# Kernel tuning notes

Hardware: AMD Instinct MI355X
Metric: run time of the kernel (lower is better)

The kernel has to match this reference:

```python
import jax, jax.numpy as jnp
import numpy as np

B = 8192
NUM_NODES = 100000
EMB = 128
W1D, W2D, W3D = 64, 128, 256   # witness_dims
CODE = 128
HID = 64                        # hardcoded hidden_dim in WitnessExtractor / decoder
TOTW = W1D + W2D + W3D          # 448


def _linear_params(key, fan_in, fan_out):
    k1, k2 = jax.random.split(key)
    bound = 1.0 / np.sqrt(fan_in)
    w = jax.random.uniform(k1, (fan_out, fan_in), jnp.float32, -bound, bound)
    b = jax.random.uniform(k2, (fan_out,), jnp.float32, -bound, bound)
    return w, b


def setup_inputs() -> dict:
    key = jax.random.key(0)
    ks = jax.random.split(key, 12)
    u = jax.random.randint(ks[0], (B,), 0, NUM_NODES, dtype=jnp.int64 if jax.config.jax_enable_x64 else jnp.int32)
    v = jax.random.randint(ks[1], (B,), 0, NUM_NODES, dtype=u.dtype)
    emb = jax.random.normal(ks[2], (NUM_NODES, EMB), jnp.float32)
    e1_w1, e1_b1 = _linear_params(ks[3], 2 * EMB, HID)
    e1_w2, e1_b2 = _linear_params(ks[4], HID, W1D)
    e2_w1, e2_b1 = _linear_params(ks[5], 2 * EMB + W1D, HID)
    e2_w2, e2_b2 = _linear_params(ks[6], HID, W2D)
    e3_w1, e3_b1 = _linear_params(ks[7], 2 * EMB + W2D, HID)
    e3_w2, e3_b2 = _linear_params(ks[8], HID, W3D)
    trop_w = jax.random.normal(ks[9], (CODE, TOTW), jnp.float32)  # init_scale=1.0
    dec_w1, dec_b1 = _linear_params(ks[10], CODE, HID)
    dec_w2, dec_b2 = _linear_params(ks[11], HID, 1)
    return dict(u=u, v=v, emb=emb,
                e1_w1=e1_w1, e1_b1=e1_b1, e1_w2=e1_w2, e1_b2=e1_b2,
                e2_w1=e2_w1, e2_b1=e2_b1, e2_w2=e2_w2, e2_b2=e2_b2,
                e3_w1=e3_w1, e3_b1=e3_b1, e3_w2=e3_w2, e3_b2=e3_b2,
                trop_w=trop_w, dec_w1=dec_w1, dec_b1=dec_b1,
                dec_w2=dec_w2, dec_b2=dec_b2)


def _witness(x, w1, b1, w2, b2):
    h = jax.nn.relu(x @ w1.T + b1)
    return jax.nn.sigmoid(h @ w2.T + b2)


def reference(u, v, emb,
              e1_w1, e1_b1, e1_w2, e1_b2,
              e2_w1, e2_b1, e2_w2, e2_b2,
              e3_w1, e3_b1, e3_w2, e3_b2,
              trop_w, dec_w1, dec_b1, dec_w2, dec_b2):
    u_emb = emb[u]                               # [B, EMB]
    v_emb = emb[v]
    base = jnp.concatenate([u_emb, v_emb], axis=1)  # [B, 2*EMB]
    w1 = _witness(base, e1_w1, e1_b1, e1_w2, e1_b2)
    w2 = _witness(jnp.concatenate([base, w1], axis=1), e2_w1, e2_b1, e2_w2, e2_b2)
    w3 = _witness(jnp.concatenate([base, w2], axis=1), e3_w1, e3_b1, e3_w2, e3_b2)
    wit = jnp.concatenate([w1, w2, w3], axis=1)  # [B, TOTW]
    # tropical (min-plus) matmul: code[b,o] = min_j (wit[b,j] + trop_w[o,j])
    code = jnp.min(wit[:, None, :] + trop_w[None, :, :], axis=2)  # [B, CODE]
    h = jax.nn.relu(code @ dec_w1.T + dec_b1)
    return h @ dec_w2.T + dec_b2                 # [B, 1]
```

## Files before the change

kernel.cpp:

```cpp
#include <hip/hip_runtime.h>
#include <hip/hip_fp16.h>
#include <math.h>

#define BATCH 8192
#define EMB 128
#define TILE 32
#define NTHREADS 1024
#define NWAVES 16

#define OFF_E1W1 0
#define OFF_E1W2 16384
#define OFF_E2W1 20480
#define OFF_E2W2 40960
#define OFF_E3W1 49152
#define OFF_E3W2 73728
#define OFF_TROP 90112
#define OFF_DW1  147456
#define OFF_DW2  155648
#define W_TOTAL  155712

typedef __attribute__((ext_vector_type(8))) _Float16 v8h;
typedef __attribute__((ext_vector_type(2))) _Float16 half2v;
typedef __attribute__((ext_vector_type(4))) float v4f;

struct Smem {
    _Float16 XB[32 * 32 * 8];
    _Float16 WIT[56 * 32 * 8];
    _Float16 H[8 * 32 * 8];
    _Float16 CODE[16 * 32 * 8];
};

static_assert(sizeof(Smem) == (32*32*8 + 56*32*8 + 8*32*8 + 16*32*8) * 2, "lds size");

__global__ __launch_bounds__(256) void cvt_weights_kernel(
    const float* __restrict__ s0, const float* __restrict__ s1,
    const float* __restrict__ s2, const float* __restrict__ s3,
    const float* __restrict__ s4, const float* __restrict__ s5,
    const float* __restrict__ s6, const float* __restrict__ s7,
    const float* __restrict__ s8, _Float16* __restrict__ ws)
{
    const int idx4 = (blockIdx.x * 256 + threadIdx.x) * 4;
    if (idx4 >= W_TOTAL) return;
    const float* src; int off;
    if      (idx4 < OFF_E1W2) { src = s0; off = OFF_E1W1; }
    else if (idx4 < OFF_E2W1) { src = s1; off = OFF_E1W2; }
    else if (idx4 < OFF_E2W2) { src = s2; off = OFF_E2W1; }
    else if (idx4 < OFF_E3W1) { src = s3; off = OFF_E2W2; }
    else if (idx4 < OFF_E3W2) { src = s4; off = OFF_E3W1; }
    else if (idx4 < OFF_TROP) { src = s5; off = OFF_E3W2; }
    else if (idx4 < OFF_DW1)  { src = s6; off = OFF_TROP; }
    else if (idx4 < OFF_DW2)  { src = s7; off = OFF_DW1;  }
    else                      { src = s8; off = OFF_DW2;  }
    const float4 v = *(const float4*)(src + (idx4 - off));
    _Float16* dst = ws + idx4;
    dst[0] = (_Float16)v.x;
    dst[1] = (_Float16)v.y;
    dst[2] = (_Float16)v.z;
    dst[3] = (_Float16)v.w;
}

template <int K, int STEPS0, int O, int ACT>
__device__ __forceinline__ void dense_mfma(
    const _Float16* __restrict__ Wg, const float* __restrict__ bias,
    const _Float16* A0, const _Float16* A1, _Float16* Out,
    int wave, int lane)
{
    constexpr int STEPS = K / 32;
    constexpr int NJOBS = 2 * (O / 16);
    constexpr int JLIM = (NJOBS < NWAVES) ? NWAVES : NJOBS;
    const int l15 = lane & 15;
    const int quad = lane >> 4;

    for (int job = wave; job < JLIM; job += NWAVES) {
        const int jid = job % NJOBS;
        const int mt = jid & 1;
        const int nt = jid >> 1;
        v4f c = {0.f, 0.f, 0.f, 0.f};
        const _Float16* wrow = Wg + (size_t)(nt * 16 + l15) * K + quad * 8;
        #pragma unroll
        for (int s = 0; s < STEPS; ++s) {
            const int g = s * 4 + quad;
            const _Float16* asrc = (s < STEPS0)
                ? (A0 + ((size_t)g * 32 + mt * 16 + l15) * 8)
                : (A1 + ((size_t)(g - STEPS0 * 4) * 32 + mt * 16 + l15) * 8);
            const v8h a = *(const v8h*)asrc;
            const v8h b = *(const v8h*)(wrow + s * 32);
            c = __builtin_amdgcn_mfma_f32_16x16x32_f16(a, b, c, 0, 0, 0);
        }
        const int o = nt * 16 + l15;
        const float bs = bias[o];
        #pragma unroll
        for (int i = 0; i < 4; ++i) {
            float vv = c[i] + bs;
            if (ACT == 0) vv = fmaxf(vv, 0.f);
            else          vv = 1.f / (1.f + __expf(-vv));
            const int m = mt * 16 + quad * 4 + i;
            Out[((o >> 3) * 32 + m) * 8 + (o & 7)] = (_Float16)vv;
        }
    }
}

__global__ __launch_bounds__(NTHREADS) void tacit_fused_kernel(
    const int* __restrict__ u, const int* __restrict__ v,
    const float* __restrict__ emb,
    const float* __restrict__ e1_b1, const float* __restrict__ e1_b2,
    const float* __restrict__ e2_b1, const float* __restrict__ e2_b2,
    const float* __restrict__ e3_b1, const float* __restrict__ e3_b2,
    const float* __restrict__ dec_b1, const float* __restrict__ dec_b2,
    const _Float16* __restrict__ ws,
    float* __restrict__ out)
{
    __shared__ Smem S;
    const int tid = threadIdx.x;
    const int lane = tid & 63;
    const int wave = tid >> 6;
    const int row0 = blockIdx.x * TILE;

    {
        const int row = tid & 31;
        const int kq = tid >> 5;
        const int node = (kq < 16) ? u[row0 + row] : v[row0 + row];
        const int col = (kq & 15) * 8;
        const float4 f0 = *(const float4*)(emb + (size_t)node * EMB + col);
        const float4 f1 = *(const float4*)(emb + (size_t)node * EMB + col + 4);
        v8h hv;
        hv[0] = (_Float16)f0.x; hv[1] = (_Float16)f0.y;
        hv[2] = (_Float16)f0.z; hv[3] = (_Float16)f0.w;
        hv[4] = (_Float16)f1.x; hv[5] = (_Float16)f1.y;
        hv[6] = (_Float16)f1.z; hv[7] = (_Float16)f1.w;
        *(v8h*)&S.XB[((size_t)kq * 32 + row) * 8] = hv;
    }
    __syncthreads();

    dense_mfma<256, 8, 64, 0>(ws + OFF_E1W1, e1_b1, S.XB, nullptr, S.H, wave, lane);
    __syncthreads();
    dense_mfma<64, 2, 64, 1>(ws + OFF_E1W2, e1_b2, S.H, nullptr, S.WIT, wave, lane);
    __syncthreads();

    dense_mfma<320, 8, 64, 0>(ws + OFF_E2W1, e2_b1, S.XB, S.WIT, S.H, wave, lane);
    __syncthreads();
    dense_mfma<64, 2, 128, 1>(ws + OFF_E2W2, e2_b2, S.H, nullptr, S.WIT + 8 * 256, wave, lane);
    __syncthreads();

    dense_mfma<384, 8, 64, 0>(ws + OFF_E3W1, e3_b1, S.XB, S.WIT + 8 * 256, S.H, wave, lane);
    __syncthreads();
    dense_mfma<64, 2, 256, 1>(ws + OFF_E3W2, e3_b2, S.H, nullptr, S.WIT + 24 * 256, wave, lane);
    __syncthreads();

    {
        const int g = wave >> 1;
        const int rh = wave & 1;
        const int l15 = lane & 15;
        const int sub = lane >> 4;
        const int o = g * 16 + l15;
        half2v acc[16];
        const half2v big = {(_Float16)60000.f, (_Float16)60000.f};
        #pragma unroll
        for (int r = 0; r < 16; ++r) acc[r] = big;
        const _Float16* Trow = ws + OFF_TROP + (size_t)o * 448 + sub * 112;
        #pragma unroll 2
        for (int c = 0; c < 14; ++c) {
            const float4 wr = *(const float4*)(Trow + c * 8);
            const half2v w0 = __builtin_bit_cast(half2v, wr.x);
            const half2v w1 = __builtin_bit_cast(half2v, wr.y);
            const half2v w2 = __builtin_bit_cast(half2v, wr.z);
            const half2v w3 = __builtin_bit_cast(half2v, wr.w);
            const int kq = sub * 14 + c;
            const _Float16* xb = &S.WIT[((size_t)kq * 32 + rh * 16) * 8];
            #pragma unroll
            for (int r = 0; r < 16; ++r) {
                const float4 xr = *(const float4*)(xb + r * 8);
                half2v t0 = __builtin_bit_cast(half2v, xr.x) + w0;
                half2v t1 = __builtin_bit_cast(half2v, xr.y) + w1;
                half2v t2 = __builtin_bit_cast(half2v, xr.z) + w2;
                half2v t3 = __builtin_bit_cast(half2v, xr.w) + w3;
                t0 = __builtin_elementwise_min(t0, t1);
                t2 = __builtin_elementwise_min(t2, t3);
                acc[r] = __builtin_elementwise_min(acc[r], __builtin_elementwise_min(t0, t2));
            }
        }
        #pragma unroll
        for (int r = 0; r < 16; ++r) {
            half2v v1 = __builtin_bit_cast(half2v,
                __shfl_xor(__builtin_bit_cast(int, acc[r]), 16, 64));
            acc[r] = __builtin_elementwise_min(acc[r], v1);
            half2v v2 = __builtin_bit_cast(half2v,
                __shfl_xor(__builtin_bit_cast(int, acc[r]), 32, 64));
            acc[r] = __builtin_elementwise_min(acc[r], v2);
        }
        if (sub == 0) {
            #pragma unroll
            for (int r = 0; r < 16; ++r) {
                const _Float16 lo = acc[r].x;
                const _Float16 hi = acc[r].y;
                S.CODE[((o >> 3) * 32 + rh * 16 + r) * 8 + (o & 7)] =
                    (lo < hi) ? lo : hi;
            }
        }
    }
    __syncthreads();

    dense_mfma<128, 4, 64, 0>(ws + OFF_DW1, dec_b1, S.CODE, nullptr, S.H, wave, lane);
    __syncthreads();

    if (tid < TILE) {
        const int r = tid;
        float s = dec_b2[0];
        const _Float16* w2 = ws + OFF_DW2;
        #pragma unroll
        for (int c = 0; c < 8; ++c) {
            const float4 hr = *(const float4*)(&S.H[((size_t)c * 32 + r) * 8]);
            const float4 wr = *(const float4*)(w2 + c * 8);
            s = __builtin_amdgcn_fdot2(__builtin_bit_cast(half2v, hr.x), __builtin_bit_cast(half2v, wr.x), s, false);
            s = __builtin_amdgcn_fdot2(__builtin_bit_cast(half2v, hr.y), __builtin_bit_cast(half2v, wr.y), s, false);
            s = __builtin_amdgcn_fdot2(__builtin_bit_cast(half2v, hr.z), __builtin_bit_cast(half2v, wr.z), s, false);
            s = __builtin_amdgcn_fdot2(__builtin_bit_cast(half2v, hr.w), __builtin_bit_cast(half2v, wr.w), s, false);
        }
        out[row0 + r] = s;
    }
}

extern "C" void kernel_launch(void* const* d_in, const int* in_sizes, int n_in,
                              void* d_out, int out_size, void* d_ws, size_t ws_size,
                              hipStream_t stream) {
    const int*   u      = (const int*)d_in[0];
    const int*   v      = (const int*)d_in[1];
    const float* emb    = (const float*)d_in[2];
    const float* e1_w1  = (const float*)d_in[3];
    const float* e1_b1  = (const float*)d_in[4];
    const float* e1_w2  = (const float*)d_in[5];
    const float* e1_b2  = (const float*)d_in[6];
    const float* e2_w1  = (const float*)d_in[7];
    const float* e2_b1  = (const float*)d_in[8];
    const float* e2_w2  = (const float*)d_in[9];
    const float* e2_b2  = (const float*)d_in[10];
    const float* e3_w1  = (const float*)d_in[11];
    const float* e3_b1  = (const float*)d_in[12];
    const float* e3_w2  = (const float*)d_in[13];
    const float* e3_b2  = (const float*)d_in[14];
    const float* trop_w = (const float*)d_in[15];
    const float* dec_w1 = (const float*)d_in[16];
    const float* dec_b1 = (const float*)d_in[17];
    const float* dec_w2 = (const float*)d_in[18];
    const float* dec_b2 = (const float*)d_in[19];
    float* out = (float*)d_out;
    _Float16* ws = (_Float16*)d_ws;

    const int cvt_blocks = (W_TOTAL / 4 + 255) / 256;
    cvt_weights_kernel<<<cvt_blocks, 256, 0, stream>>>(
        e1_w1, e1_w2, e2_w1, e2_w2, e3_w1, e3_w2, trop_w, dec_w1, dec_w2, ws);

    tacit_fused_kernel<<<BATCH / TILE, NTHREADS, 0, stream>>>(
        u, v, emb,
        e1_b1, e1_b2, e2_b1, e2_b2, e3_b1, e3_b2, dec_b1, dec_b2,
        ws, out);
}
```

Baseline: 161.6 us.

## Prune tropical weights to near-minimum entries and sparsify min-plus stage

A prep kernel finds each trop_w row's minimum and keeps only entries within about 1.02 of it, stored as a compact (index, fp16 value) list with row offsets in the workspace. This is exact because the sigmoid witnesses lie in (0,1), so a pruned entry can never be the minimum. The dense min-plus loop over all 448 columns becomes a short sparse scan over a row-major witness copy in LDS. The batch tile also shrinks to 16 rows with a padded LDS stride and an occupancy hint. Risks: many waves sit idle in the small dense layers, and a fixed entry cap (4096) could truncate unusual weight sets.

```diff
diff --git a/kernel.cpp b/kernel.cpp
--- a/kernel.cpp
+++ b/kernel.cpp
@@ -4,9 +4,12 @@
 
 #define BATCH 8192
 #define EMB 128
-#define TILE 32
+#define TILE 16
 #define NTHREADS 1024
 #define NWAVES 16
+#define CH 136
+#define WITS 450
+#define ENT_CAP 4096
 
 #define OFF_E1W1 0
 #define OFF_E1W2 16384
@@ -14,78 +17,111 @@
 #define OFF_E2W2 40960
 #define OFF_E3W1 49152
 #define OFF_E3W2 73728
-#define OFF_TROP 90112
-#define OFF_DW1  147456
-#define OFF_DW2  155648
-#define W_TOTAL  155712
+#define OFF_DW1  90112
+#define OFF_DW2  98304
+#define W_DENSE  98368
 
 typedef __attribute__((ext_vector_type(8))) _Float16 v8h;
-typedef __attribute__((ext_vector_type(2))) _Float16 half2v;
 typedef __attribute__((ext_vector_type(4))) float v4f;
 
 struct Smem {
-    _Float16 XB[32 * 32 * 8];
-    _Float16 WIT[56 * 32 * 8];
-    _Float16 H[8 * 32 * 8];
-    _Float16 CODE[16 * 32 * 8];
+    _Float16 XB[32 * CH];
+    _Float16 W12C[24 * CH];
+    _Float16 H[8 * CH];
+    _Float16 CODE[16 * CH];
+    _Float16 WITrm[TILE * WITS];
+    unsigned int ent[ENT_CAP];
+    unsigned int off[132];
 };
 
-static_assert(sizeof(Smem) == (32*32*8 + 56*32*8 + 8*32*8 + 16*32*8) * 2, "lds size");
-
-__global__ __launch_bounds__(256) void cvt_weights_kernel(
+__global__ __launch_bounds__(256) void prep_kernel(
     const float* __restrict__ s0, const float* __restrict__ s1,
     const float* __restrict__ s2, const float* __restrict__ s3,
     const float* __restrict__ s4, const float* __restrict__ s5,
     const float* __restrict__ s6, const float* __restrict__ s7,
-    const float* __restrict__ s8, _Float16* __restrict__ ws)
+    const float* __restrict__ trop, _Float16* __restrict__ ws)
 {
-    const int idx4 = (blockIdx.x * 256 + threadIdx.x) * 4;
-    if (idx4 >= W_TOTAL) return;
-    const float* src; int off;
-    if      (idx4 < OFF_E1W2) { src = s0; off = OFF_E1W1; }
-    else if (idx4 < OFF_E2W1) { src = s1; off = OFF_E1W2; }
-    else if (idx4 < OFF_E2W2) { src = s2; off = OFF_E2W1; }
-    else if (idx4 < OFF_E3W1) { src = s3; off = OFF_E2W2; }
-    else if (idx4 < OFF_E3W2) { src = s4; off = OFF_E3W1; }
-    else if (idx4 < OFF_TROP) { src = s5; off = OFF_E3W2; }
-    else if (idx4 < OFF_DW1)  { src = s6; off = OFF_TROP; }
-    else if (idx4 < OFF_DW2)  { src = s7; off = OFF_DW1;  }
-    else                      { src = s8; off = OFF_DW2;  }
-    const float4 v = *(const float4*)(src + (idx4 - off));
-    _Float16* dst = ws + idx4;
-    dst[0] = (_Float16)v.x;
-    dst[1] = (_Float16)v.y;
-    dst[2] = (_Float16)v.z;
-    dst[3] = (_Float16)v.w;
-}
-
-template <int K, int STEPS0, int O, int ACT>
+    const int b = blockIdx.x;
+    if (b < 97) {
+        const int idx4 = (b * 256 + (int)threadIdx.x) * 4;
+        if (idx4 >= W_DENSE) return;
+        const float* src; int off;
+        if      (idx4 < OFF_E1W2) { src = s0; off = OFF_E1W1; }
+        else if (idx4 < OFF_E2W1) { src = s1; off = OFF_E1W2; }
+        else if (idx4 < OFF_E2W2) { src = s2; off = OFF_E2W1; }
+        else if (idx4 < OFF_E3W1) { src = s3; off = OFF_E2W2; }
+        else if (idx4 < OFF_E3W2) { src = s4; off = OFF_E3W1; }
+        else if (idx4 < OFF_DW1)  { src = s5; off = OFF_E3W2; }
+        else if (idx4 < OFF_DW2)  { src = s6; off = OFF_DW1;  }
+        else                      { src = s7; off = OFF_DW2;  }
+        const float4 v = *(const float4*)(src + (idx4 - off));
+        _Float16* dst = ws + idx4;
+        dst[0] = (_Float16)v.x; dst[1] = (_Float16)v.y;
+        dst[2] = (_Float16)v.z; dst[3] = (_Float16)v.w;
+    } else {
+        __shared__ unsigned int cnt[128];
+        __shared__ unsigned int offs[129];
+        const int o = threadIdx.x;
+        float mn = 1e30f;
+        float thr = 0.f;
+        if (o < 128) {
+            const float* row = trop + (size_t)o * 448;
+            for (int j = 0; j < 448; j += 4) {
+                const float4 t = *(const float4*)(row + j);
+                mn = fminf(mn, fminf(fminf(t.x, t.y), fminf(t.z, t.w)));
+            }
+            thr = mn + 1.02f;
+            int n = 0;
+            for (int j = 0; j < 448; ++j) n += (row[j] <= thr) ? 1 : 0;
+            cnt[o] = (unsigned)n;
+        }
+        __syncthreads();
+        if (threadIdx.x == 0) {
+            unsigned int s = 0;
+            for (int i = 0; i < 128; ++i) { offs[i] = s; s += cnt[i]; }
+            offs[128] = s;
+        }
+        __syncthreads();
+        unsigned int* base = (unsigned int*)(ws + W_DENSE);
+        if (o < 129) base[o] = offs[o < 128 ? o : 128];
+        if (o < 128) {
+            const float* row = trop + (size_t)o * 448;
+            unsigned int w = 132 + offs[o];
+            for (int j = 0; j < 448; ++j) {
+                const float t = row[j];
+                if (t <= thr && w < 132 + ENT_CAP) {
+                    const unsigned short hb =
+                        __builtin_bit_cast(unsigned short, (_Float16)t);
+                    base[w++] = ((unsigned)j << 16) | hb;
+                }
+            }
+        }
+    }
+}
+
+template <int K, int STEPS0, int O, int ACT, bool CHUNKW, bool RMW>
 __device__ __forceinline__ void dense_mfma(
     const _Float16* __restrict__ Wg, const float* __restrict__ bias,
-    const _Float16* A0, const _Float16* A1, _Float16* Out,
-    int wave, int lane)
+    const _Float16* A0, const _Float16* A1,
+    _Float16* OutC, _Float16* OutRM, int rmbase, int wave, int lane)
 {
     constexpr int STEPS = K / 32;
-    constexpr int NJOBS = 2 * (O / 16);
-    constexpr int JLIM = (NJOBS < NWAVES) ? NWAVES : NJOBS;
+    constexpr int NJOBS = O / 16;
     const int l15 = lane & 15;
     const int quad = lane >> 4;
 
-    for (int job = wave; job < JLIM; job += NWAVES) {
-        const int jid = job % NJOBS;
-        const int mt = jid & 1;
-        const int nt = jid >> 1;
+    for (int nt = wave; nt < NJOBS; nt += NWAVES) {
         v4f c = {0.f, 0.f, 0.f, 0.f};
         const _Float16* wrow = Wg + (size_t)(nt * 16 + l15) * K + quad * 8;
         #pragma unroll
         for (int s = 0; s < STEPS; ++s) {
             const int g = s * 4 + quad;
             const _Float16* asrc = (s < STEPS0)
-                ? (A0 + ((size_t)g * 32 + mt * 16 + l15) * 8)
-                : (A1 + ((size_t)(g - STEPS0 * 4) * 32 + mt * 16 + l15) * 8);
+                ? (A0 + g * CH + l15 * 8)
+                : (A1 + (g - STEPS0 * 4) * CH + l15 * 8);
             const v8h a = *(const v8h*)asrc;
-            const v8h b = *(const v8h*)(wrow + s * 32);
-            c = __builtin_amdgcn_mfma_f32_16x16x32_f16(a, b, c, 0, 0, 0);
+            const v8h bfr = *(const v8h*)(wrow + s * 32);
+            c = __builtin_amdgcn_mfma_f32_16x16x32_f16(a, bfr, c, 0, 0, 0);
         }
         const int o = nt * 16 + l15;
         const float bs = bias[o];
@@ -94,13 +130,15 @@
             float vv = c[i] + bs;
             if (ACT == 0) vv = fmaxf(vv, 0.f);
             else          vv = 1.f / (1.f + __expf(-vv));
-            const int m = mt * 16 + quad * 4 + i;
-            Out[((o >> 3) * 32 + m) * 8 + (o & 7)] = (_Float16)vv;
-        }
-    }
-}
-
-__global__ __launch_bounds__(NTHREADS) void tacit_fused_kernel(
+            const int m = quad * 4 + i;
+            const _Float16 hv = (_Float16)vv;
+            if (CHUNKW) OutC[(o >> 3) * CH + m * 8 + (o & 7)] = hv;
+            if (RMW)    OutRM[m * WITS + rmbase + o] = hv;
+        }
+    }
+}
+
+__global__ __launch_bounds__(NTHREADS, 8) void tacit_fused_kernel(
     const int* __restrict__ u, const int* __restrict__ v,
     const float* __restrict__ emb,
     const float* __restrict__ e1_b1, const float* __restrict__ e1_b2,
@@ -116,9 +154,9 @@
     const int wave = tid >> 6;
     const int row0 = blockIdx.x * TILE;
 
-    {
-        const int row = tid & 31;
-        const int kq = tid >> 5;
+    if (tid < 512) {
+        const int row = tid & 15;
+        const int kq = tid >> 4;
         const int node = (kq < 16) ? u[row0 + row] : v[row0 + row];
         const int col = (kq & 15) * 8;
         const float4 f0 = *(const float4*)(emb + (size_t)node * EMB + col);
@@ -128,79 +166,63 @@
         hv[2] = (_Float16)f0.z; hv[3] = (_Float16)f0.w;
         hv[4] = (_Float16)f1.x; hv[5] = (_Float16)f1.y;
         hv[6] = (_Float16)f1.z; hv[7] = (_Float16)f1.w;
-        *(v8h*)&S.XB[((size_t)kq * 32 + row) * 8] = hv;
-    }
-    __syncthreads();
-
-    dense_mfma<256, 8, 64, 0>(ws + OFF_E1W1, e1_b1, S.XB, nullptr, S.H, wave, lane);
-    __syncthreads();
-    dense_mfma<64, 2, 64, 1>(ws + OFF_E1W2, e1_b2, S.H, nullptr, S.WIT, wave, lane);
-    __syncthreads();
-
-    dense_mfma<320, 8, 64, 0>(ws + OFF_E2W1, e2_b1, S.XB, S.WIT, S.H, wave, lane);
-    __syncthreads();
-    dense_mfma<64, 2, 128, 1>(ws + OFF_E2W2, e2_b2, S.H, nullptr, S.WIT + 8 * 256, wave, lane);
-    __syncthreads();
-
-    dense_mfma<384, 8, 64, 0>(ws + OFF_E3W1, e3_b1, S.XB, S.WIT + 8 * 256, S.H, wave, lane);
-    __syncthreads();
-    dense_mfma<64, 2, 256, 1>(ws + OFF_E3W2, e3_b2, S.H, nullptr, S.WIT + 24 * 256, wave, lane);
-    __syncthreads();
-
+        *(v8h*)&S.XB[kq * CH + row * 8] = hv;
+    }
     {
-        const int g = wave >> 1;
-        const int rh = wave & 1;
-        const int l15 = lane & 15;
-        const int sub = lane >> 4;
-        const int o = g * 16 + l15;
-        half2v acc[16];
-        const half2v big = {(_Float16)60000.f, (_Float16)60000.f};
-        #pragma unroll
-        for (int r = 0; r < 16; ++r) acc[r] = big;
-        const _Float16* Trow = ws + OFF_TROP + (size_t)o * 448 + sub * 112;
-        #pragma unroll 2
-        for (int c = 0; c < 14; ++c) {
-            const float4 wr = *(const float4*)(Trow + c * 8);
-            const half2v w0 = __builtin_bit_cast(half2v, wr.x);
-            const half2v w1 = __builtin_bit_cast(half2v, wr.y);
-            const half2v w2 = __builtin_bit_cast(half2v, wr.z);
-            const half2v w3 = __builtin_bit_cast(half2v, wr.w);
-            const int kq = sub * 14 + c;
-            const _Float16* xb = &S.WIT[((size_t)kq * 32 + rh * 16) * 8];
-            #pragma unroll
-            for (int r = 0; r < 16; ++r) {
-                const float4 xr = *(const float4*)(xb + r * 8);
-                half2v t0 = __builtin_bit_cast(half2v, xr.x) + w0;
-                half2v t1 = __builtin_bit_cast(half2v, xr.y) + w1;
-                half2v t2 = __builtin_bit_cast(half2v, xr.z) + w2;
-                half2v t3 = __builtin_bit_cast(half2v, xr.w) + w3;
-                t0 = __builtin_elementwise_min(t0, t1);
-                t2 = __builtin_elementwise_min(t2, t3);
-                acc[r] = __builtin_elementwise_min(acc[r], __builtin_elementwise_min(t0, t2));
+        const unsigned int* base = (const unsigned int*)(ws + W_DENSE);
+        if (tid < 33) *(uint4*)&S.off[tid * 4] = *(const uint4*)(base + tid * 4);
+        *(uint4*)&S.ent[tid * 4] = *(const uint4*)(base + 132 + tid * 4);
+    }
+    __syncthreads();
+
+    dense_mfma<256, 8, 64, 0, true, false>(ws + OFF_E1W1, e1_b1, S.XB, nullptr,
+                                           S.H, nullptr, 0, wave, lane);
+    __syncthreads();
+    dense_mfma<64, 2, 64, 1, true, true>(ws + OFF_E1W2, e1_b2, S.H, nullptr,
+                                         S.W12C, S.WITrm, 0, wave, lane);
+    __syncthreads();
+
+    dense_mfma<320, 8, 64, 0, true, false>(ws + OFF_E2W1, e2_b1, S.XB, S.W12C,
+                                           S.H, nullptr, 0, wave, lane);
+    __syncthreads();
+    dense_mfma<64, 2, 128, 1, true, true>(ws + OFF_E2W2, e2_b2, S.H, nullptr,
+                                          S.W12C + 8 * CH, S.WITrm, 64, wave, lane);
+    __syncthreads();
+
+    dense_mfma<384, 8, 64, 0, true, false>(ws + OFF_E3W1, e3_b1, S.XB, S.W12C + 8 * CH,
+                                           S.H, nullptr, 0, wave, lane);
+    __syncthreads();
+    dense_mfma<64, 2, 256, 1, false, true>(ws + OFF_E3W2, e3_b2, S.H, nullptr,
+                                           nullptr, S.WITrm, 192, wave, lane);
+    __syncthreads();
+
+    {
+        const int r = lane & 15;
+        const int cp = lane >> 4;
+        const _Float16* wrow = &S.WITrm[r * WITS];
+        #pragma unroll
+        for (int i = 0; i < 8; ++i) {
+            const int o = (wave << 3) + i;
+            const int beg = (int)S.off[o];
+            const int end = (int)S.off[o + 1];
+            float acc = 1e30f;
+            for (int idx = beg + cp; idx < end; idx += 4) {
+                const unsigned int cwv = S.ent[idx];
+                const int j = (int)(cwv >> 16);
+                const float tv = (float)__builtin_bit_cast(
+                    _Float16, (unsigned short)(cwv & 0xffffu));
+                acc = fminf(acc, (float)wrow[j] + tv);
             }
-        }
-        #pragma unroll
-        for (int r = 0; r < 16; ++r) {
-            half2v v1 = __builtin_bit_cast(half2v,
-                __shfl_xor(__builtin_bit_cast(int, acc[r]), 16, 64));
-            acc[r] = __builtin_elementwise_min(acc[r], v1);
-            half2v v2 = __builtin_bit_cast(half2v,
-                __shfl_xor(__builtin_bit_cast(int, acc[r]), 32, 64));
-            acc[r] = __builtin_elementwise_min(acc[r], v2);
-        }
-        if (sub == 0) {
-            #pragma unroll
-            for (int r = 0; r < 16; ++r) {
-                const _Float16 lo = acc[r].x;
-                const _Float16 hi = acc[r].y;
-                S.CODE[((o >> 3) * 32 + rh * 16 + r) * 8 + (o & 7)] =
-                    (lo < hi) ? lo : hi;
-            }
-        }
-    }
-    __syncthreads();
-
-    dense_mfma<128, 4, 64, 0>(ws + OFF_DW1, dec_b1, S.CODE, nullptr, S.H, wave, lane);
+            acc = fminf(acc, __shfl_xor(acc, 16, 64));
+            acc = fminf(acc, __shfl_xor(acc, 32, 64));
+            if (cp == 0)
+                S.CODE[(o >> 3) * CH + r * 8 + (o & 7)] = (_Float16)acc;
+        }
+    }
+    __syncthreads();
+
+    dense_mfma<128, 4, 64, 0, true, false>(ws + OFF_DW1, dec_b1, S.CODE, nullptr,
+                                           S.H, nullptr, 0, wave, lane);
     __syncthreads();
 
     if (tid < TILE) {
@@ -209,12 +231,10 @@
         const _Float16* w2 = ws + OFF_DW2;
         #pragma unroll
         for (int c = 0; c < 8; ++c) {
-            const float4 hr = *(const float4*)(&S.H[((size_t)c * 32 + r) * 8]);
-            const float4 wr = *(const float4*)(w2 + c * 8);
-            s = __builtin_amdgcn_fdot2(__builtin_bit_cast(half2v, hr.x), __builtin_bit_cast(half2v, wr.x), s, false);
-            s = __builtin_amdgcn_fdot2(__builtin_bit_cast(half2v, hr.y), __builtin_bit_cast(half2v, wr.y), s, false);
-            s = __builtin_amdgcn_fdot2(__builtin_bit_cast(half2v, hr.z), __builtin_bit_cast(half2v, wr.z), s, false);
-            s = __builtin_amdgcn_fdot2(__builtin_bit_cast(half2v, hr.w), __builtin_bit_cast(half2v, wr.w), s, false);
+            const v8h hr = *(const v8h*)(&S.H[c * CH + r * 8]);
+            const v8h wr = *(const v8h*)(w2 + c * 8);
+            #pragma unroll
+            for (int t = 0; t < 8; ++t) s += (float)hr[t] * (float)wr[t];
         }
         out[row0 + r] = s;
     }
@@ -246,9 +266,8 @@
     float* out = (float*)d_out;
     _Float16* ws = (_Float16*)d_ws;
 
-    const int cvt_blocks = (W_TOTAL / 4 + 255) / 256;
-    cvt_weights_kernel<<<cvt_blocks, 256, 0, stream>>>(
-        e1_w1, e1_w2, e2_w1, e2_w2, e3_w1, e3_w2, trop_w, dec_w1, dec_w2, ws);
+    prep_kernel<<<98, 256, 0, stream>>>(
+        e1_w1, e1_w2, e2_w1, e2_w2, e3_w1, e3_w2, dec_w1, dec_w2, trop_w, ws);
 
     tacit_fused_kernel<<<BATCH / TILE, NTHREADS, 0, stream>>>(
         u, v, emb,
```

Result: slower. 230.5 us (+42.7%).
